# Kernel optimization log

Hardware: AMD Instinct MI355X
Metric: run time of the kernel (lower is better)

## Reference

```python
import jax, jax.numpy as jnp
import numpy as np

TOP_K = 2
NUM_EXPERTS = 64


def setup_inputs() -> dict:
    key = jax.random.key(0)
    k1, k2, k3 = jax.random.split(key, 3)
    T, D, E = 16384, 2048, NUM_EXPERTS
    x = jax.random.normal(k1, (T, D), dtype=jnp.float32)
    # gate projection weight (the _forward of the concrete router)
    w_gate = jax.random.normal(k2, (D, E), dtype=jnp.float32) * (1.0 / np.sqrt(D))
    # gate.perturbation(scores.shape, NORMAL): additive Gaussian noise, materialized for determinism
    noise = jax.random.normal(k3, (T, E), dtype=jnp.float32)
    return {"x": x, "w_gate": w_gate, "noise": noise}


def reference(x, w_gate, noise):
    T, E = x.shape[0], w_gate.shape[1]
    # _forward: expert scores [T, E]
    scores = x @ w_gate
    # gate.compute on perturbed scores: softmax -> top-k -> renormalized gates
    probs = jax.nn.softmax(scores + noise, axis=-1)
    topk_vals, topk_idx = jax.lax.top_k(probs, TOP_K)          # [T, k]
    gates = topk_vals / jnp.sum(topk_vals, axis=-1, keepdims=True)
    # combine tensor [T, E]: gate weight scattered to the chosen experts
    rows = jnp.arange(T)[:, None]                               # [T, 1]
    combine = jnp.zeros((T, E), dtype=gates.dtype).at[rows, topk_idx].add(gates)
    # _track_expert_activations: scatter_add of ones per selected expert column
    expert_activation = jnp.zeros((E,), dtype=jnp.float32).at[topk_idx.ravel()].add(1.0)
    return combine, topk_idx, gates, expert_activation
```

## Files before the change

kernel.cpp:

```cpp
#include <hip/hip_runtime.h>
#include <math.h>

#define T_TOKENS 16384
#define DIM      2048
#define NEXP     64
#define TOPK     2

#define OFF_COMBINE 0
#define OFF_IDX     (T_TOKENS * NEXP)
#define OFF_GATES   (OFF_IDX + T_TOKENS * TOPK)
#define OFF_ACT     (OFF_GATES + T_TOKENS * TOPK)

#define WT_PLANE (NEXP * DIM)

#define BT    32
#define BK    32
#define NSTEP (DIM / BK)

typedef __attribute__((ext_vector_type(8))) short  short8;
typedef __attribute__((ext_vector_type(4))) float  f32x4;

#define MFMA16(a, b, c) __builtin_amdgcn_mfma_f32_16x16x32_bf16((a), (b), (c), 0, 0, 0)

__device__ __align__(16) unsigned short g_wt[3 * WT_PLANE];

__global__ void wsplit_kernel(const float* __restrict__ w,
                              float* __restrict__ out) {
    const int tid = threadIdx.x;
    const int e   = blockIdx.x;
    if (e == 0 && tid < NEXP) out[OFF_ACT + tid] = 0.0f;

    const int k0 = tid * 8;
    short8 hs, ms, ls;
    #pragma unroll
    for (int i = 0; i < 8; ++i) {
        const float v = w[(size_t)(k0 + i) * NEXP + e];
        const unsigned int bv = __builtin_bit_cast(unsigned int, v);
        const unsigned int hb = bv & 0xFFFF0000u;
        const float r1 = v - __builtin_bit_cast(float, hb);
        const unsigned int r1b = __builtin_bit_cast(unsigned int, r1);
        const unsigned int mb = r1b & 0xFFFF0000u;
        const float r2 = r1 - __builtin_bit_cast(float, mb);
        const unsigned int lb = __builtin_bit_cast(unsigned int, r2);
        hs[i] = (short)(hb >> 16);
        ms[i] = (short)(mb >> 16);
        ls[i] = (short)(lb >> 16);
    }
    *reinterpret_cast<short8*>(&g_wt[(size_t)e * DIM + k0])                = hs;
    *reinterpret_cast<short8*>(&g_wt[(size_t)e * DIM + k0 + WT_PLANE])     = ms;
    *reinterpret_cast<short8*>(&g_wt[(size_t)e * DIM + k0 + 2 * WT_PLANE]) = ls;
}

__device__ __forceinline__ void gload_lds16(const void* g, void* s) {
    __builtin_amdgcn_global_load_lds(
        (const __attribute__((address_space(1))) void*)g,
        (__attribute__((address_space(3))) void*)s, 16, 0, 0);
}

__device__ __forceinline__ void split8(const float4 a, const float4 b,
                                       short8& ah, short8& am, short8& al) {
    float v[8] = {a.x, a.y, a.z, a.w, b.x, b.y, b.z, b.w};
    #pragma unroll
    for (int i = 0; i < 8; ++i) {
        const unsigned int bv = __builtin_bit_cast(unsigned int, v[i]);
        const unsigned int hb = bv & 0xFFFF0000u;
        const float r1 = v[i] - __builtin_bit_cast(float, hb);
        const unsigned int r1b = __builtin_bit_cast(unsigned int, r1);
        const unsigned int mb = r1b & 0xFFFF0000u;
        const float r2 = r1 - __builtin_bit_cast(float, mb);
        const unsigned int lb = __builtin_bit_cast(unsigned int, r2);
        ah[i] = (short)(hb >> 16);
        am[i] = (short)(mb >> 16);
        al[i] = (short)(lb >> 16);
    }
}

__global__ __launch_bounds__(256, 2)
void router_kernel(const float* __restrict__ x,
                   const float* __restrict__ noise,
                   float* __restrict__ out) {
    __shared__ __align__(16) float          aS[2][BT * BK];
    __shared__ __align__(16) unsigned short wS[2][3 * NEXP * BK];
    __shared__ float scores[BT][68];
    __shared__ float nshs[BT][68];
    __shared__ float g1s[BT], g2s[BT];
    __shared__ int   i1s[BT], i2s[BT];
    __shared__ float bins[NEXP];

    const int tid  = threadIdx.x;
    const int l    = tid & 63;
    const int wv   = __builtin_amdgcn_readfirstlane(tid >> 6);
    const int lrow = l & 15;
    const int lk   = l >> 4;
    const int brow = blockIdx.x * BT;

    if (tid < NEXP) bins[tid] = 0.0f;

    #pragma unroll
    for (int i = 0; i < 2; ++i) {
        const int idx = tid + i * 256;
        const int r = idx >> 4, c = (idx & 15) * 4;
        *reinterpret_cast<float4*>(&nshs[r][c]) =
            *reinterpret_cast<const float4*>(noise + (size_t)(brow + r) * NEXP + c);
    }

    const int arow = wv * 8 + (l >> 3);
    const int agch = ((l & 7) - arow) & 7;
    const float* asrc = x + (size_t)(brow + arow) * DIM + agch * 4;
    float* adst = &aS[0][0] + wv * 256;

    const unsigned short* wsrc[3];
    unsigned short* wdst[3];
    #pragma unroll
    for (int t = 0; t < 3; ++t) {
        const int op = wv * 3 + t;
        const int p  = op >> 2, q = op & 3;
        const int e  = q * 16 + (l >> 2);
        const int gch = ((l & 3) - e) & 3;
        wsrc[t] = g_wt + (size_t)p * WT_PLANE + (size_t)e * DIM + gch * 8;
        wdst[t] = &wS[0][0] + p * 2048 + q * 512;
    }

#define STAGE(bf, ss) do {                                            \
        gload_lds16(asrc + (ss) * BK,     adst    + (bf) * 1024);     \
        gload_lds16(wsrc[0] + (ss) * BK,  wdst[0] + (bf) * 6144);     \
        gload_lds16(wsrc[1] + (ss) * BK,  wdst[1] + (bf) * 6144);     \
        gload_lds16(wsrc[2] + (ss) * BK,  wdst[2] + (bf) * 6144);     \
    } while (0)

    const int af = wv & 1;
    const int n0 = (wv >> 1) * 2;
    const int ar = af * 16 + lrow;
    const int ac0 = ((2 * lk + ar) & 7) * 4;
    const int ac1 = ((2 * lk + 1 + ar) & 7) * 4;
    int woff[2];
    #pragma unroll
    for (int n = 0; n < 2; ++n) {
        const int e = (n0 + n) * 16 + lrow;
        woff[n] = e * 32 + ((lk + e) & 3) * 8;
    }

    f32x4 acc[2];
    acc[0] = (f32x4){0.f, 0.f, 0.f, 0.f};
    acc[1] = acc[0];

    STAGE(0, 0);
    __syncthreads();

    #pragma unroll 2
    for (int s = 0; s < NSTEP; ++s) {
        const int b = s & 1;
        const int sn = (s + 1 < NSTEP) ? (s + 1) : s;
        STAGE(b ^ 1, sn);

        const float* ab = &aS[b][ar * 32];
        const float4 xa0 = *reinterpret_cast<const float4*>(ab + ac0);
        const float4 xa1 = *reinterpret_cast<const float4*>(ab + ac1);
        short8 ah, am, al;
        split8(xa0, xa1, ah, am, al);

        const unsigned short* wbuf = &wS[b][0];
        #pragma unroll
        for (int n = 0; n < 2; ++n) {
            const short8 Wh = *reinterpret_cast<const short8*>(wbuf +        woff[n]);
            const short8 Wm = *reinterpret_cast<const short8*>(wbuf + 2048 + woff[n]);
            const short8 Wl = *reinterpret_cast<const short8*>(wbuf + 4096 + woff[n]);
            acc[n] = MFMA16(ah, Wh, acc[n]);
            acc[n] = MFMA16(ah, Wm, acc[n]);
            acc[n] = MFMA16(am, Wh, acc[n]);
            acc[n] = MFMA16(ah, Wl, acc[n]);
            acc[n] = MFMA16(am, Wm, acc[n]);
            acc[n] = MFMA16(al, Wh, acc[n]);
        }
        __syncthreads();
    }
#undef STAGE

    #pragma unroll
    for (int n = 0; n < 2; ++n)
        #pragma unroll
        for (int j = 0; j < 4; ++j)
            scores[af * 16 + lk * 4 + j][(n0 + n) * 16 + lrow] = acc[n][j];
    __syncthreads();

    if (tid < BT) {
        const int r   = tid;
        const int row = brow + r;
        float m1 = -1e30f, m2 = -1e30f;
        int i1 = 0, i2 = 0;
        #pragma unroll
        for (int j = 0; j < NEXP; j += 4) {
            float4 s4       = *reinterpret_cast<const float4*>(&scores[r][j]);
            const float4 nv = *reinterpret_cast<const float4*>(&nshs[r][j]);
            s4.x += nv.x; s4.y += nv.y; s4.z += nv.z; s4.w += nv.w;
            if (s4.x > m1) { m2 = m1; i2 = i1; m1 = s4.x; i1 = j + 0; } else if (s4.x > m2) { m2 = s4.x; i2 = j + 0; }
            if (s4.y > m1) { m2 = m1; i2 = i1; m1 = s4.y; i1 = j + 1; } else if (s4.y > m2) { m2 = s4.y; i2 = j + 1; }
            if (s4.z > m1) { m2 = m1; i2 = i1; m1 = s4.z; i1 = j + 2; } else if (s4.z > m2) { m2 = s4.z; i2 = j + 2; }
            if (s4.w > m1) { m2 = m1; i2 = i1; m1 = s4.w; i1 = j + 3; } else if (s4.w > m2) { m2 = s4.w; i2 = j + 3; }
        }

        const float t  = expf(m2 - m1);
        const float g1 = 1.0f / (1.0f + t);
        const float g2 = 1.0f - g1;

        out[OFF_IDX + row * 2 + 0]   = (float)i1;
        out[OFF_IDX + row * 2 + 1]   = (float)i2;
        out[OFF_GATES + row * 2 + 0] = g1;
        out[OFF_GATES + row * 2 + 1] = g2;

        g1s[r] = g1; g2s[r] = g2; i1s[r] = i1; i2s[r] = i2;
        atomicAdd(&bins[i1], 1.0f);
        atomicAdd(&bins[i2], 1.0f);
    }
    __syncthreads();

    #pragma unroll
    for (int i = 0; i < 2; ++i) {
        const int idx = tid + i * 256;
        const int r = idx >> 4, c = (idx & 15) * 4;
        const int   a  = i1s[r], b = i2s[r];
        const float ga = g1s[r], gb = g2s[r];
        float4 v;
        v.x = (c + 0 == a) ? ga : (c + 0 == b) ? gb : 0.0f;
        v.y = (c + 1 == a) ? ga : (c + 1 == b) ? gb : 0.0f;
        v.z = (c + 2 == a) ? ga : (c + 2 == b) ? gb : 0.0f;
        v.w = (c + 3 == a) ? ga : (c + 3 == b) ? gb : 0.0f;
        *reinterpret_cast<float4*>(
            out + OFF_COMBINE + (size_t)(brow + r) * NEXP + c) = v;
    }

    if (tid < NEXP) {
        const float v = bins[tid];
        if (v != 0.0f) atomicAdd(out + OFF_ACT + tid, v);
    }
}

extern "C" void kernel_launch(void* const* d_in, const int* in_sizes, int n_in,
                              void* d_out, int out_size, void* d_ws, size_t ws_size,
                              hipStream_t stream) {
    const float* x     = (const float*)d_in[0];
    const float* wg    = (const float*)d_in[1];
    const float* noise = (const float*)d_in[2];
    float* out = (float*)d_out;

    wsplit_kernel<<<NEXP, 256, 0, stream>>>(wg, out);
    router_kernel<<<T_TOKENS / BT, 256, 0, stream>>>(x, noise, out);
}
```

Measured before the change: 255.5 us.

## Split K across blocks with LDS-resident weight chunks and separate reduce kernel

Replaces the single fused router kernel with a split-K score kernel and a separate reduction kernel. Each score block keeps one 256-wide K chunk of the three bf16 weight planes resident in 160KB of LDS and streams many 16-token x tiles through it, so weights are no longer re-fetched from global memory for every 32-token block. Partial scores for all 8 chunks go to a global scratch buffer, and a reduce kernel sums them, adds noise and performs top-2, gating and the combine/activation writes. This adds an extra launch and a 32MB partial write/read round trip, and the score kernel runs only 256 blocks at one block per CU with a blocking vmcnt(0) wait per tile, so load latency is not overlapped.

```diff
diff --git a/kernel.cpp b/kernel.cpp
--- a/kernel.cpp
+++ b/kernel.cpp
@@ -11,18 +11,23 @@
 #define OFF_GATES   (OFF_IDX + T_TOKENS * TOPK)
 #define OFF_ACT     (OFF_GATES + T_TOKENS * TOPK)
 
-#define WT_PLANE (NEXP * DIM)
-
-#define BT    32
-#define BK    32
-#define NSTEP (DIM / BK)
+#define CHUNKS 8
+#define CK     256
+#define CSTEPS (CK / 32)
+#define PLANE_SHORTS (NEXP * CK)
+#define WCH_SHORTS   (3 * PLANE_SHORTS)
+
+#define LDS_A_WAVE 16384
+#define LDS_W_BASE 65536
+#define LDS_TOTAL  163840
 
 typedef __attribute__((ext_vector_type(8))) short  short8;
 typedef __attribute__((ext_vector_type(4))) float  f32x4;
 
 #define MFMA16(a, b, c) __builtin_amdgcn_mfma_f32_16x16x32_bf16((a), (b), (c), 0, 0, 0)
 
-__device__ __align__(16) unsigned short g_wt[3 * WT_PLANE];
+__device__ __align__(16) unsigned short g_wt3[CHUNKS * WCH_SHORTS];
+__device__ __align__(16) float g_part[CHUNKS * T_TOKENS * NEXP];
 
 __global__ void wsplit_kernel(const float* __restrict__ w,
                               float* __restrict__ out) {
@@ -30,7 +35,9 @@
     const int e   = blockIdx.x;
     if (e == 0 && tid < NEXP) out[OFF_ACT + tid] = 0.0f;
 
-    const int k0 = tid * 8;
+    const int k0    = tid * 8;
+    const int chunk = k0 >> 8;
+    const int kin   = k0 & 255;
     short8 hs, ms, ls;
     #pragma unroll
     for (int i = 0; i < 8; ++i) {
@@ -46,9 +53,10 @@
         ms[i] = (short)(mb >> 16);
         ls[i] = (short)(lb >> 16);
     }
-    *reinterpret_cast<short8*>(&g_wt[(size_t)e * DIM + k0])                = hs;
-    *reinterpret_cast<short8*>(&g_wt[(size_t)e * DIM + k0 + WT_PLANE])     = ms;
-    *reinterpret_cast<short8*>(&g_wt[(size_t)e * DIM + k0 + 2 * WT_PLANE]) = ls;
+    unsigned short* dst = g_wt3 + (size_t)chunk * WCH_SHORTS + e * CK + kin;
+    *reinterpret_cast<short8*>(dst)                    = hs;
+    *reinterpret_cast<short8*>(dst + PLANE_SHORTS)     = ms;
+    *reinterpret_cast<short8*>(dst + 2 * PLANE_SHORTS) = ls;
 }
 
 __device__ __forceinline__ void gload_lds16(const void* g, void* s) {
@@ -75,124 +83,138 @@
     }
 }
 
-__global__ __launch_bounds__(256, 2)
-void router_kernel(const float* __restrict__ x,
-                   const float* __restrict__ noise,
-                   float* __restrict__ out) {
-    __shared__ __align__(16) float          aS[2][BT * BK];
-    __shared__ __align__(16) unsigned short wS[2][3 * NEXP * BK];
-    __shared__ float scores[BT][68];
-    __shared__ float nshs[BT][68];
-    __shared__ float g1s[BT], g2s[BT];
-    __shared__ int   i1s[BT], i2s[BT];
-    __shared__ float bins[NEXP];
+__global__ __launch_bounds__(256, 1)
+void score_kernel(const float* __restrict__ x) {
+    __shared__ __align__(16) unsigned char lds[LDS_TOTAL];
 
     const int tid  = threadIdx.x;
     const int l    = tid & 63;
     const int wv   = __builtin_amdgcn_readfirstlane(tid >> 6);
     const int lrow = l & 15;
     const int lk   = l >> 4;
-    const int brow = blockIdx.x * BT;
+    const int chunk = blockIdx.x & 7;
+    const int tg    = blockIdx.x >> 3;
+    const int tok0  = tg * 512;
+
+    {
+        const unsigned short* src = g_wt3 + (size_t)chunk * WCH_SHORTS;
+        #pragma unroll 4
+        for (int r = 0; r < 24; ++r) {
+            const int idx = tid + r * 256;
+            const short8 v = *reinterpret_cast<const short8*>(src + idx * 8);
+            const int p   = idx >> 11;
+            const int rem = idx & 2047;
+            const int e   = rem >> 5;
+            const int s   = rem & 31;
+            *reinterpret_cast<short8*>(
+                lds + LDS_W_BASE + p * 32768 + e * 512 + ((s ^ (e & 7)) * 16)) = v;
+        }
+    }
+    __syncthreads();
+
+    unsigned char* aw = lds + wv * LDS_A_WAVE;
+
+    #pragma unroll 1
+    for (int ti = 0; ti < 8; ++ti) {
+        const int tile0 = tok0 + (wv * 8 + ti) * 16;
+
+        #pragma unroll
+        for (int o = 0; o < 16; ++o) {
+            const float* src = x + (size_t)(tile0 + o) * DIM + chunk * CK
+                                 + ((l ^ (o & 7)) << 2);
+            gload_lds16(src, aw + o * 1024);
+        }
+        asm volatile("s_waitcnt vmcnt(0)" ::: "memory");
+        __builtin_amdgcn_sched_barrier(0);
+
+        f32x4 acc[4];
+        #pragma unroll
+        for (int n = 0; n < 4; ++n) acc[n] = (f32x4){0.f, 0.f, 0.f, 0.f};
+
+        #pragma unroll
+        for (int s = 0; s < CSTEPS; ++s) {
+            const int g0 = s * 8 + 2 * lk;
+            const float4 xa0 = *reinterpret_cast<const float4*>(
+                aw + lrow * 1024 + ((g0 ^ (lrow & 7)) * 16));
+            const float4 xa1 = *reinterpret_cast<const float4*>(
+                aw + lrow * 1024 + (((g0 + 1) ^ (lrow & 7)) * 16));
+            short8 ah, am, al;
+            split8(xa0, xa1, ah, am, al);
+
+            const int ws = s * 4 + lk;
+            #pragma unroll
+            for (int n = 0; n < 4; ++n) {
+                const int e = n * 16 + lrow;
+                const unsigned char* wb =
+                    lds + LDS_W_BASE + e * 512 + ((ws ^ (e & 7)) * 16);
+                const short8 Wh = *reinterpret_cast<const short8*>(wb);
+                const short8 Wm = *reinterpret_cast<const short8*>(wb + 32768);
+                const short8 Wl = *reinterpret_cast<const short8*>(wb + 65536);
+                acc[n] = MFMA16(ah, Wh, acc[n]);
+                acc[n] = MFMA16(ah, Wm, acc[n]);
+                acc[n] = MFMA16(am, Wh, acc[n]);
+                acc[n] = MFMA16(ah, Wl, acc[n]);
+                acc[n] = MFMA16(am, Wm, acc[n]);
+                acc[n] = MFMA16(al, Wh, acc[n]);
+            }
+        }
+
+        float* pb = g_part + ((size_t)chunk * T_TOKENS + tile0) * NEXP;
+        #pragma unroll
+        for (int n = 0; n < 4; ++n)
+            #pragma unroll
+            for (int j = 0; j < 4; ++j)
+                pb[(lk * 4 + j) * NEXP + n * 16 + lrow] = acc[n][j];
+    }
+}
+
+__global__ __launch_bounds__(256, 2)
+void reduce_kernel(const float* __restrict__ noise,
+                   float* __restrict__ out) {
+    __shared__ float scores[64][68];
+    __shared__ float g1s[64], g2s[64];
+    __shared__ int   i1s[64], i2s[64];
+    __shared__ float bins[NEXP];
+
+    const int tid  = threadIdx.x;
+    const int brow = blockIdx.x * 64;
+    const int r    = tid >> 2;
+    const int q    = tid & 3;
 
     if (tid < NEXP) bins[tid] = 0.0f;
 
-    #pragma unroll
-    for (int i = 0; i < 2; ++i) {
-        const int idx = tid + i * 256;
-        const int r = idx >> 4, c = (idx & 15) * 4;
-        *reinterpret_cast<float4*>(&nshs[r][c]) =
-            *reinterpret_cast<const float4*>(noise + (size_t)(brow + r) * NEXP + c);
-    }
-
-    const int arow = wv * 8 + (l >> 3);
-    const int agch = ((l & 7) - arow) & 7;
-    const float* asrc = x + (size_t)(brow + arow) * DIM + agch * 4;
-    float* adst = &aS[0][0] + wv * 256;
-
-    const unsigned short* wsrc[3];
-    unsigned short* wdst[3];
-    #pragma unroll
-    for (int t = 0; t < 3; ++t) {
-        const int op = wv * 3 + t;
-        const int p  = op >> 2, q = op & 3;
-        const int e  = q * 16 + (l >> 2);
-        const int gch = ((l & 3) - e) & 3;
-        wsrc[t] = g_wt + (size_t)p * WT_PLANE + (size_t)e * DIM + gch * 8;
-        wdst[t] = &wS[0][0] + p * 2048 + q * 512;
-    }
-
-#define STAGE(bf, ss) do {                                            \
-        gload_lds16(asrc + (ss) * BK,     adst    + (bf) * 1024);     \
-        gload_lds16(wsrc[0] + (ss) * BK,  wdst[0] + (bf) * 6144);     \
-        gload_lds16(wsrc[1] + (ss) * BK,  wdst[1] + (bf) * 6144);     \
-        gload_lds16(wsrc[2] + (ss) * BK,  wdst[2] + (bf) * 6144);     \
-    } while (0)
-
-    const int af = wv & 1;
-    const int n0 = (wv >> 1) * 2;
-    const int ar = af * 16 + lrow;
-    const int ac0 = ((2 * lk + ar) & 7) * 4;
-    const int ac1 = ((2 * lk + 1 + ar) & 7) * 4;
-    int woff[2];
-    #pragma unroll
-    for (int n = 0; n < 2; ++n) {
-        const int e = (n0 + n) * 16 + lrow;
-        woff[n] = e * 32 + ((lk + e) & 3) * 8;
-    }
-
-    f32x4 acc[2];
-    acc[0] = (f32x4){0.f, 0.f, 0.f, 0.f};
-    acc[1] = acc[0];
-
-    STAGE(0, 0);
+    {
+        const int c0 = q * 16;
+        float4 s0 = *reinterpret_cast<const float4*>(noise + (size_t)(brow + r) * NEXP + c0);
+        float4 s1 = *reinterpret_cast<const float4*>(noise + (size_t)(brow + r) * NEXP + c0 + 4);
+        float4 s2 = *reinterpret_cast<const float4*>(noise + (size_t)(brow + r) * NEXP + c0 + 8);
+        float4 s3 = *reinterpret_cast<const float4*>(noise + (size_t)(brow + r) * NEXP + c0 + 12);
+        #pragma unroll
+        for (int c = 0; c < CHUNKS; ++c) {
+            const float* pb = g_part + ((size_t)c * T_TOKENS + brow + r) * NEXP + c0;
+            const float4 p0 = *reinterpret_cast<const float4*>(pb);
+            const float4 p1 = *reinterpret_cast<const float4*>(pb + 4);
+            const float4 p2 = *reinterpret_cast<const float4*>(pb + 8);
+            const float4 p3 = *reinterpret_cast<const float4*>(pb + 12);
+            s0.x += p0.x; s0.y += p0.y; s0.z += p0.z; s0.w += p0.w;
+            s1.x += p1.x; s1.y += p1.y; s1.z += p1.z; s1.w += p1.w;
+            s2.x += p2.x; s2.y += p2.y; s2.z += p2.z; s2.w += p2.w;
+            s3.x += p3.x; s3.y += p3.y; s3.z += p3.z; s3.w += p3.w;
+        }
+        *reinterpret_cast<float4*>(&scores[r][c0])      = s0;
+        *reinterpret_cast<float4*>(&scores[r][c0 + 4])  = s1;
+        *reinterpret_cast<float4*>(&scores[r][c0 + 8])  = s2;
+        *reinterpret_cast<float4*>(&scores[r][c0 + 12]) = s3;
+    }
     __syncthreads();
 
-    #pragma unroll 2
-    for (int s = 0; s < NSTEP; ++s) {
-        const int b = s & 1;
-        const int sn = (s + 1 < NSTEP) ? (s + 1) : s;
-        STAGE(b ^ 1, sn);
-
-        const float* ab = &aS[b][ar * 32];
-        const float4 xa0 = *reinterpret_cast<const float4*>(ab + ac0);
-        const float4 xa1 = *reinterpret_cast<const float4*>(ab + ac1);
-        short8 ah, am, al;
-        split8(xa0, xa1, ah, am, al);
-
-        const unsigned short* wbuf = &wS[b][0];
-        #pragma unroll
-        for (int n = 0; n < 2; ++n) {
-            const short8 Wh = *reinterpret_cast<const short8*>(wbuf +        woff[n]);
-            const short8 Wm = *reinterpret_cast<const short8*>(wbuf + 2048 + woff[n]);
-            const short8 Wl = *reinterpret_cast<const short8*>(wbuf + 4096 + woff[n]);
-            acc[n] = MFMA16(ah, Wh, acc[n]);
-            acc[n] = MFMA16(ah, Wm, acc[n]);
-            acc[n] = MFMA16(am, Wh, acc[n]);
-            acc[n] = MFMA16(ah, Wl, acc[n]);
-            acc[n] = MFMA16(am, Wm, acc[n]);
-            acc[n] = MFMA16(al, Wh, acc[n]);
-        }
-        __syncthreads();
-    }
-#undef STAGE
-
-    #pragma unroll
-    for (int n = 0; n < 2; ++n)
-        #pragma unroll
-        for (int j = 0; j < 4; ++j)
-            scores[af * 16 + lk * 4 + j][(n0 + n) * 16 + lrow] = acc[n][j];
-    __syncthreads();
-
-    if (tid < BT) {
-        const int r   = tid;
-        const int row = brow + r;
+    if (tid < 64) {
+        const int row = brow + tid;
         float m1 = -1e30f, m2 = -1e30f;
         int i1 = 0, i2 = 0;
         #pragma unroll
         for (int j = 0; j < NEXP; j += 4) {
-            float4 s4       = *reinterpret_cast<const float4*>(&scores[r][j]);
-            const float4 nv = *reinterpret_cast<const float4*>(&nshs[r][j]);
-            s4.x += nv.x; s4.y += nv.y; s4.z += nv.z; s4.w += nv.w;
+            const float4 s4 = *reinterpret_cast<const float4*>(&scores[tid][j]);
             if (s4.x > m1) { m2 = m1; i2 = i1; m1 = s4.x; i1 = j + 0; } else if (s4.x > m2) { m2 = s4.x; i2 = j + 0; }
             if (s4.y > m1) { m2 = m1; i2 = i1; m1 = s4.y; i1 = j + 1; } else if (s4.y > m2) { m2 = s4.y; i2 = j + 1; }
             if (s4.z > m1) { m2 = m1; i2 = i1; m1 = s4.z; i1 = j + 2; } else if (s4.z > m2) { m2 = s4.z; i2 = j + 2; }
@@ -208,25 +230,25 @@
         out[OFF_GATES + row * 2 + 0] = g1;
         out[OFF_GATES + row * 2 + 1] = g2;
 
-        g1s[r] = g1; g2s[r] = g2; i1s[r] = i1; i2s[r] = i2;
+        g1s[tid] = g1; g2s[tid] = g2; i1s[tid] = i1; i2s[tid] = i2;
         atomicAdd(&bins[i1], 1.0f);
         atomicAdd(&bins[i2], 1.0f);
     }
     __syncthreads();
 
     #pragma unroll
-    for (int i = 0; i < 2; ++i) {
+    for (int i = 0; i < 4; ++i) {
         const int idx = tid + i * 256;
-        const int r = idx >> 4, c = (idx & 15) * 4;
-        const int   a  = i1s[r], b = i2s[r];
-        const float ga = g1s[r], gb = g2s[r];
+        const int rr = idx >> 4, c = (idx & 15) * 4;
+        const int   a  = i1s[rr], b = i2s[rr];
+        const float ga = g1s[rr], gb = g2s[rr];
         float4 v;
         v.x = (c + 0 == a) ? ga : (c + 0 == b) ? gb : 0.0f;
         v.y = (c + 1 == a) ? ga : (c + 1 == b) ? gb : 0.0f;
         v.z = (c + 2 == a) ? ga : (c + 2 == b) ? gb : 0.0f;
         v.w = (c + 3 == a) ? ga : (c + 3 == b) ? gb : 0.0f;
         *reinterpret_cast<float4*>(
-            out + OFF_COMBINE + (size_t)(brow + r) * NEXP + c) = v;
+            out + OFF_COMBINE + (size_t)(brow + rr) * NEXP + c) = v;
     }
 
     if (tid < NEXP) {
@@ -244,5 +266,6 @@
     float* out = (float*)d_out;
 
     wsplit_kernel<<<NEXP, 256, 0, stream>>>(wg, out);
-    router_kernel<<<T_TOKENS / BT, 256, 0, stream>>>(x, noise, out);
-}
+    score_kernel<<<CHUNKS * 32, 256, 0, stream>>>(x);
+    reduce_kernel<<<T_TOKENS / 64, 256, 0, stream>>>(noise, out);
+}
```

Measured after the change: 228.5 us. 1.12x faster.

## Enlarge router tile to 64 tokens and BK 64 with chunked swizzled weight layout

Applied to the files above, without the earlier changes.

Doubles the per-block token tile to 64 rows with 512 threads and doubles the K step to 64. This halves how often each block re-reads the three bf16 weight planes and halves the number of barrier-separated iterations. The weight split kernel now writes the planes in per-K-chunk contiguous blocks, so each stage is one contiguous copy. XOR swizzles are used for the LDS layout of both operands. The cost is one 512-thread block per CU with a larger 80KB LDS footprint, and less latency hiding from independent blocks.

```diff
diff --git a/kernel.cpp b/kernel.cpp
--- a/kernel.cpp
+++ b/kernel.cpp
@@ -11,18 +11,21 @@
 #define OFF_GATES   (OFF_IDX + T_TOKENS * TOPK)
 #define OFF_ACT     (OFF_GATES + T_TOKENS * TOPK)
 
-#define WT_PLANE (NEXP * DIM)
-
-#define BT    32
-#define BK    32
-#define NSTEP (DIM / BK)
+#define BK      64
+#define NITER   (DIM / BK)
+#define WCH_SH  (3 * NEXP * BK)
+
+#define A_BUF_B 16384
+#define W_BASE  32768
+#define W_BUF_B 24576
+#define LDS_B   81920
 
 typedef __attribute__((ext_vector_type(8))) short  short8;
 typedef __attribute__((ext_vector_type(4))) float  f32x4;
 
 #define MFMA16(a, b, c) __builtin_amdgcn_mfma_f32_16x16x32_bf16((a), (b), (c), 0, 0, 0)
 
-__device__ __align__(16) unsigned short g_wt[3 * WT_PLANE];
+__device__ __align__(16) unsigned short g_wt3[NITER * WCH_SH];
 
 __global__ void wsplit_kernel(const float* __restrict__ w,
                               float* __restrict__ out) {
@@ -30,7 +33,9 @@
     const int e   = blockIdx.x;
     if (e == 0 && tid < NEXP) out[OFF_ACT + tid] = 0.0f;
 
-    const int k0 = tid * 8;
+    const int k0    = tid * 8;
+    const int chunk = tid >> 3;
+    const int kin   = (tid & 7) * 8;
     short8 hs, ms, ls;
     #pragma unroll
     for (int i = 0; i < 8; ++i) {
@@ -46,9 +51,10 @@
         ms[i] = (short)(mb >> 16);
         ls[i] = (short)(lb >> 16);
     }
-    *reinterpret_cast<short8*>(&g_wt[(size_t)e * DIM + k0])                = hs;
-    *reinterpret_cast<short8*>(&g_wt[(size_t)e * DIM + k0 + WT_PLANE])     = ms;
-    *reinterpret_cast<short8*>(&g_wt[(size_t)e * DIM + k0 + 2 * WT_PLANE]) = ls;
+    unsigned short* dst = g_wt3 + (size_t)chunk * WCH_SH + e * BK + kin;
+    *reinterpret_cast<short8*>(dst)            = hs;
+    *reinterpret_cast<short8*>(dst + NEXP*BK)  = ms;
+    *reinterpret_cast<short8*>(dst + 2*NEXP*BK)= ls;
 }
 
 __device__ __forceinline__ void gload_lds16(const void* g, void* s) {
@@ -75,70 +81,52 @@
     }
 }
 
-__global__ __launch_bounds__(256, 2)
+__global__ __launch_bounds__(512, 1)
 void router_kernel(const float* __restrict__ x,
                    const float* __restrict__ noise,
                    float* __restrict__ out) {
-    __shared__ __align__(16) float          aS[2][BT * BK];
-    __shared__ __align__(16) unsigned short wS[2][3 * NEXP * BK];
-    __shared__ float scores[BT][68];
-    __shared__ float nshs[BT][68];
-    __shared__ float g1s[BT], g2s[BT];
-    __shared__ int   i1s[BT], i2s[BT];
-    __shared__ float bins[NEXP];
+    __shared__ __align__(16) unsigned char lds[LDS_B];
 
     const int tid  = threadIdx.x;
     const int l    = tid & 63;
     const int wv   = __builtin_amdgcn_readfirstlane(tid >> 6);
     const int lrow = l & 15;
     const int lk   = l >> 4;
-    const int brow = blockIdx.x * BT;
-
-    if (tid < NEXP) bins[tid] = 0.0f;
-
-    #pragma unroll
-    for (int i = 0; i < 2; ++i) {
-        const int idx = tid + i * 256;
-        const int r = idx >> 4, c = (idx & 15) * 4;
-        *reinterpret_cast<float4*>(&nshs[r][c]) =
-            *reinterpret_cast<const float4*>(noise + (size_t)(brow + r) * NEXP + c);
-    }
-
-    const int arow = wv * 8 + (l >> 3);
-    const int agch = ((l & 7) - arow) & 7;
-    const float* asrc = x + (size_t)(brow + arow) * DIM + agch * 4;
-    float* adst = &aS[0][0] + wv * 256;
-
+    const int mt   = wv >> 1;
+    const int nh   = wv & 1;
+    const int brow = blockIdx.x * 64;
+
+    const float* asrc[2];
+    int adst[2];
+    #pragma unroll
+    for (int t = 0; t < 2; ++t) {
+        const int op = wv * 2 + t;
+        const int ro = op * 4 + (l >> 4);
+        asrc[t] = x + (size_t)(brow + ro) * DIM + (((l & 15) ^ (ro & 15)) << 2);
+        adst[t] = op * 1024;
+    }
     const unsigned short* wsrc[3];
-    unsigned short* wdst[3];
+    int wdst[3];
     #pragma unroll
     for (int t = 0; t < 3; ++t) {
-        const int op = wv * 3 + t;
-        const int p  = op >> 2, q = op & 3;
-        const int e  = q * 16 + (l >> 2);
-        const int gch = ((l & 3) - e) & 3;
-        wsrc[t] = g_wt + (size_t)p * WT_PLANE + (size_t)e * DIM + gch * 8;
-        wdst[t] = &wS[0][0] + p * 2048 + q * 512;
-    }
-
-#define STAGE(bf, ss) do {                                            \
-        gload_lds16(asrc + (ss) * BK,     adst    + (bf) * 1024);     \
-        gload_lds16(wsrc[0] + (ss) * BK,  wdst[0] + (bf) * 6144);     \
-        gload_lds16(wsrc[1] + (ss) * BK,  wdst[1] + (bf) * 6144);     \
-        gload_lds16(wsrc[2] + (ss) * BK,  wdst[2] + (bf) * 6144);     \
+        const int w = wv * 3 + t;
+        const int p = w >> 3, q = w & 7;
+        const int e = q * 8 + (l >> 3);
+        wsrc[t] = g_wt3 + p * (NEXP * BK) + e * BK + (((l & 7) ^ (e & 7)) << 3);
+        wdst[t] = W_BASE + p * 8192 + q * 1024;
+    }
+
+#define STAGE(bf, it) do {                                                    \
+        gload_lds16(asrc[0] + (it) * BK, lds + (bf) * A_BUF_B + adst[0]);     \
+        gload_lds16(asrc[1] + (it) * BK, lds + (bf) * A_BUF_B + adst[1]);     \
+        gload_lds16(wsrc[0] + (size_t)(it) * WCH_SH, lds + (bf) * W_BUF_B + wdst[0]); \
+        gload_lds16(wsrc[1] + (size_t)(it) * WCH_SH, lds + (bf) * W_BUF_B + wdst[1]); \
+        gload_lds16(wsrc[2] + (size_t)(it) * WCH_SH, lds + (bf) * W_BUF_B + wdst[2]); \
     } while (0)
 
-    const int af = wv & 1;
-    const int n0 = (wv >> 1) * 2;
-    const int ar = af * 16 + lrow;
-    const int ac0 = ((2 * lk + ar) & 7) * 4;
-    const int ac1 = ((2 * lk + 1 + ar) & 7) * 4;
-    int woff[2];
-    #pragma unroll
-    for (int n = 0; n < 2; ++n) {
-        const int e = (n0 + n) * 16 + lrow;
-        woff[n] = e * 32 + ((lk + e) & 3) * 8;
-    }
+    const int arow = mt * 16 + lrow;
+    const int e0   = (nh * 2 + 0) * 16 + lrow;
+    const int e1   = (nh * 2 + 1) * 16 + lrow;
 
     f32x4 acc[2];
     acc[0] = (f32x4){0.f, 0.f, 0.f, 0.f};
@@ -148,42 +136,78 @@
     __syncthreads();
 
     #pragma unroll 2
-    for (int s = 0; s < NSTEP; ++s) {
-        const int b = s & 1;
-        const int sn = (s + 1 < NSTEP) ? (s + 1) : s;
-        STAGE(b ^ 1, sn);
-
-        const float* ab = &aS[b][ar * 32];
-        const float4 xa0 = *reinterpret_cast<const float4*>(ab + ac0);
-        const float4 xa1 = *reinterpret_cast<const float4*>(ab + ac1);
-        short8 ah, am, al;
-        split8(xa0, xa1, ah, am, al);
-
-        const unsigned short* wbuf = &wS[b][0];
+    for (int it = 0; it < NITER; ++it) {
+        const int b  = it & 1;
+        const int tn = (it + 1 < NITER) ? (it + 1) : it;
+        STAGE(b ^ 1, tn);
+
+        const unsigned char* ab = lds + b * A_BUF_B + arow * 256;
+        const unsigned char* w0 = lds + b * W_BUF_B + W_BASE + e0 * 128;
+        const unsigned char* w1 = lds + b * W_BUF_B + W_BASE + e1 * 128;
+
         #pragma unroll
-        for (int n = 0; n < 2; ++n) {
-            const short8 Wh = *reinterpret_cast<const short8*>(wbuf +        woff[n]);
-            const short8 Wm = *reinterpret_cast<const short8*>(wbuf + 2048 + woff[n]);
-            const short8 Wl = *reinterpret_cast<const short8*>(wbuf + 4096 + woff[n]);
-            acc[n] = MFMA16(ah, Wh, acc[n]);
-            acc[n] = MFMA16(ah, Wm, acc[n]);
-            acc[n] = MFMA16(am, Wh, acc[n]);
-            acc[n] = MFMA16(ah, Wl, acc[n]);
-            acc[n] = MFMA16(am, Wm, acc[n]);
-            acc[n] = MFMA16(al, Wh, acc[n]);
+        for (int s = 0; s < 2; ++s) {
+            const int g0 = s * 8 + 2 * lk;
+            const float4 xa0 = *reinterpret_cast<const float4*>(
+                ab + (((g0)     ^ (arow & 15)) << 4));
+            const float4 xa1 = *reinterpret_cast<const float4*>(
+                ab + (((g0 + 1) ^ (arow & 15)) << 4));
+            short8 ah, am, al;
+            split8(xa0, xa1, ah, am, al);
+
+            const int ws = s * 4 + lk;
+            const int o0 = ((ws ^ (e0 & 7)) << 4);
+            const int o1 = ((ws ^ (e1 & 7)) << 4);
+            const short8 Wh0 = *reinterpret_cast<const short8*>(w0 + o0);
+            const short8 Wm0 = *reinterpret_cast<const short8*>(w0 + 8192 + o0);
+            const short8 Wl0 = *reinterpret_cast<const short8*>(w0 + 16384 + o0);
+            const short8 Wh1 = *reinterpret_cast<const short8*>(w1 + o1);
+            const short8 Wm1 = *reinterpret_cast<const short8*>(w1 + 8192 + o1);
+            const short8 Wl1 = *reinterpret_cast<const short8*>(w1 + 16384 + o1);
+
+            acc[0] = MFMA16(ah, Wh0, acc[0]);
+            acc[0] = MFMA16(ah, Wm0, acc[0]);
+            acc[0] = MFMA16(am, Wh0, acc[0]);
+            acc[0] = MFMA16(ah, Wl0, acc[0]);
+            acc[0] = MFMA16(am, Wm0, acc[0]);
+            acc[0] = MFMA16(al, Wh0, acc[0]);
+            acc[1] = MFMA16(ah, Wh1, acc[1]);
+            acc[1] = MFMA16(ah, Wm1, acc[1]);
+            acc[1] = MFMA16(am, Wh1, acc[1]);
+            acc[1] = MFMA16(ah, Wl1, acc[1]);
+            acc[1] = MFMA16(am, Wm1, acc[1]);
+            acc[1] = MFMA16(al, Wh1, acc[1]);
         }
         __syncthreads();
     }
 #undef STAGE
+
+    float (*scores)[68] = reinterpret_cast<float (*)[68]>(lds);
+    float (*nsh)[68]    = reinterpret_cast<float (*)[68]>(lds + 17408);
+    float* g1s  = reinterpret_cast<float*>(lds + 34816);
+    float* g2s  = g1s + 64;
+    int*   i1s  = reinterpret_cast<int*>(g2s + 64);
+    int*   i2s  = i1s + 64;
+    float* bins = reinterpret_cast<float*>(i2s + 64);
 
     #pragma unroll
     for (int n = 0; n < 2; ++n)
         #pragma unroll
         for (int j = 0; j < 4; ++j)
-            scores[af * 16 + lk * 4 + j][(n0 + n) * 16 + lrow] = acc[n][j];
+            scores[mt * 16 + lk * 4 + j][(nh * 2 + n) * 16 + lrow] = acc[n][j];
+
+    if (tid < NEXP) bins[tid] = 0.0f;
+
+    #pragma unroll
+    for (int i = 0; i < 2; ++i) {
+        const int idx = tid + i * 512;
+        const int r = idx >> 4, c = (idx & 15) * 4;
+        *reinterpret_cast<float4*>(&nsh[r][c]) =
+            *reinterpret_cast<const float4*>(noise + (size_t)(brow + r) * NEXP + c);
+    }
     __syncthreads();
 
-    if (tid < BT) {
+    if (tid < 64) {
         const int r   = tid;
         const int row = brow + r;
         float m1 = -1e30f, m2 = -1e30f;
@@ -191,7 +215,7 @@
         #pragma unroll
         for (int j = 0; j < NEXP; j += 4) {
             float4 s4       = *reinterpret_cast<const float4*>(&scores[r][j]);
-            const float4 nv = *reinterpret_cast<const float4*>(&nshs[r][j]);
+            const float4 nv = *reinterpret_cast<const float4*>(&nsh[r][j]);
             s4.x += nv.x; s4.y += nv.y; s4.z += nv.z; s4.w += nv.w;
             if (s4.x > m1) { m2 = m1; i2 = i1; m1 = s4.x; i1 = j + 0; } else if (s4.x > m2) { m2 = s4.x; i2 = j + 0; }
             if (s4.y > m1) { m2 = m1; i2 = i1; m1 = s4.y; i1 = j + 1; } else if (s4.y > m2) { m2 = s4.y; i2 = j + 1; }
@@ -216,7 +240,7 @@
 
     #pragma unroll
     for (int i = 0; i < 2; ++i) {
-        const int idx = tid + i * 256;
+        const int idx = tid + i * 512;
         const int r = idx >> 4, c = (idx & 15) * 4;
         const int   a  = i1s[r], b = i2s[r];
         const float ga = g1s[r], gb = g2s[r];
@@ -244,5 +268,5 @@
     float* out = (float*)d_out;
 
     wsplit_kernel<<<NEXP, 256, 0, stream>>>(wg, out);
-    router_kernel<<<T_TOKENS / BT, 256, 0, stream>>>(x, noise, out);
-}
+    router_kernel<<<T_TOKENS / 64, 512, 0, stream>>>(x, noise, out);
+}
```

New measurement: 221.6 us. 13.3% less time.
